# Performance work log

Measured on AMD Instinct MI355X. Metric: run time of the kernel, lower is better.

## Reference

```python
import jax, jax.numpy as jnp
import numpy as np

B, DIM = 8, 2048          # batch, dim == N == C (forced by module's shape constraints)
NUM_HEADS = 8


def setup_inputs() -> dict:
    key = jax.random.key(0)
    k1, k2 = jax.random.split(key)
    x = jax.random.normal(k1, (B, DIM, DIM), dtype=jnp.float32)      # (B, N, C), N==C==dim
    Wq = jax.random.normal(k2, (DIM, DIM), dtype=jnp.float32) * 0.02  # Conv1d(dim,dim,1) weight, no bias
    return {"x": x, "Wq": Wq, "H": 64, "W": 32}


def reference(x, Wq, H, W):
    Bb, N, C = x.shape
    scale = (C // NUM_HEADS) ** -0.5  # qk_scale=None -> head_dim**-0.5
    # self.q: Conv1d(dim, dim, kernel_size=1) applied to x (B, N, C) -> channel axis is N
    q = jnp.einsum('oi,bil->bol', Wq, x)             # (B, N, C)
    # sr_ratio == 1: k_ = x (no spatial reduction; self.sr not constructed)
    attn = jnp.einsum('bnc,bmc->bnm', q, x) * scale  # (B, N, N)
    # self.rwmp = MaxPool1d(dim) with row length N==dim -> max over last axis, keepdim
    m = jnp.max(attn, axis=-1, keepdims=True)        # (B, N, 1)
    # self.v = AvgPool1d(dim) on x^T (B, C, N), N==dim -> mean over tokens
    v = jnp.mean(x, axis=1, keepdims=True)           # (B, 1, C)
    y = m * v                                        # (B, N, 1) @ (B, 1, C) outer product
    # .transpose(1, 2).reshape(B, N, C)  (valid since N == C)
    return jnp.swapaxes(y, 1, 2).reshape(Bb, N, C)
```

## Files before the change

kernel.cpp:

```cpp
#include <hip/hip_runtime.h>

#define DIM 2048
#define NB 8
#define NT (DIM / 64)

typedef _Float16 f16;
typedef __attribute__((ext_vector_type(8))) _Float16 f16x8;
typedef __attribute__((ext_vector_type(4))) _Float16 f16x4;
typedef __attribute__((ext_vector_type(2))) _Float16 f16x2;
typedef __attribute__((ext_vector_type(4))) float f32x4;
typedef __attribute__((ext_vector_type(4))) unsigned u32x4;

__device__ __forceinline__ unsigned fkey(float f) {
    unsigned u = __float_as_uint(f);
    return (u & 0x80000000u) ? ~u : (u | 0x80000000u);
}
__device__ __forceinline__ float fdecode(unsigned k) {
    return (k & 0x80000000u) ? __uint_as_float(k ^ 0x80000000u)
                             : __uint_as_float(~k);
}

__device__ __forceinline__ void gld_lds16(const f16* g, f16* l) {
    __builtin_amdgcn_global_load_lds(
        (const __attribute__((address_space(1))) unsigned*)g,
        (__attribute__((address_space(3))) unsigned*)l, 16, 0, 0);
}

#define BAR() asm volatile("s_barrier" ::: "memory")
#define WAITVM(N) asm volatile("s_waitcnt vmcnt(" #N ")" ::: "memory")

__global__ __launch_bounds__(256) void k_convert(const float* __restrict__ src,
                                                 f16* __restrict__ dst, int n4) {
    int i = blockIdx.x * 256 + threadIdx.x;
    if (i >= n4) return;
    f32x4 v = ((const f32x4*)src)[i];
    ((f16x4*)dst)[i] = __builtin_convertvector(v, f16x4);
}

__global__ __launch_bounds__(256) void k_prep(const float* __restrict__ x,
                                              f16* __restrict__ Xf,
                                              float* __restrict__ vsum) {
    const int b  = blockIdx.z;
    const int c0 = blockIdx.x * 1024 + threadIdx.x * 4;
    const int n0 = blockIdx.y * 64;
    const float* px = x  + ((size_t)b * DIM + n0) * DIM + c0;
    f16*         pd = Xf + ((size_t)b * DIM + n0) * DIM + c0;
    f32x4 s = (f32x4){0.f, 0.f, 0.f, 0.f};
    #pragma unroll 8
    for (int n = 0; n < 64; ++n) {
        f32x4 v = *(const f32x4*)(px + (size_t)n * DIM);
        *(f16x4*)(pd + (size_t)n * DIM) = __builtin_convertvector(v, f16x4);
        s += v;
    }
    atomicAdd(&vsum[b * DIM + c0 + 0], s.x);
    atomicAdd(&vsum[b * DIM + c0 + 1], s.y);
    atomicAdd(&vsum[b * DIM + c0 + 2], s.z);
    atomicAdd(&vsum[b * DIM + c0 + 3], s.w);
}

__global__ __launch_bounds__(256) void k_colsum(const float* __restrict__ x,
                                                float* __restrict__ vsum) {
    int b = blockIdx.z;
    int c = blockIdx.x * 256 + threadIdx.x;
    int n0 = blockIdx.y * (DIM / 8);
    const float* p = x + ((size_t)b * DIM + n0) * DIM + c;
    float s = 0.f;
    #pragma unroll 8
    for (int n = 0; n < DIM / 8; ++n) s += p[(size_t)n * DIM];
    atomicAdd(&vsum[b * DIM + c], s);
}

__device__ __forceinline__ void gemm128_core(const f16* __restrict__ A,
                                             const f16* __restrict__ Bt,
                                             int br, int bc,
                                             f16* As, f16* Bs,
                                             f32x4 acc[4][4]) {
    const int tid  = threadIdx.x;
    const int ln   = tid & 63;
    const int wv   = tid >> 6;
    const int l15  = ln & 15;
    const int quad = ln >> 4;
    const int wr   = (wv >> 1) * 64;
    const int wc   = (wv & 1) * 64;
    const int lrow = ln >> 3;
    const int lg   = (ln & 7) ^ lrow;
    const int swz  = l15 & 7;

    const f16* gA = A  + (size_t)(br * 128 + wv * 32 + lrow) * DIM + lg * 8;
    const f16* gB = Bt + (size_t)(bc * 128 + wv * 32 + lrow) * DIM + lg * 8;
    f16* lA = As + wv * 2048 + ln * 8;
    f16* lB = Bs + wv * 2048 + ln * 8;

    #pragma unroll
    for (int i = 0; i < 4; ++i)
        #pragma unroll
        for (int j = 0; j < 4; ++j)
            acc[i][j] = (f32x4){0.f, 0.f, 0.f, 0.f};

    for (int kt = 0; kt < DIM / 64; ++kt) {
        __syncthreads();
        #pragma unroll
        for (int u = 0; u < 4; ++u) {
            gld_lds16(gA + (size_t)u * 8 * DIM, lA + u * 512);
            gld_lds16(gB + (size_t)u * 8 * DIM, lB + u * 512);
        }
        gA += 64; gB += 64;
        __syncthreads();
        #pragma unroll
        for (int kk = 0; kk < 2; ++kk) {
            const int s = (kk * 4 + quad) ^ swz;
            f16x8 af[4], bf[4];
            #pragma unroll
            for (int i = 0; i < 4; ++i)
                af[i] = *(const f16x8*)(As + (wr + i * 16 + l15) * 64 + s * 8);
            #pragma unroll
            for (int j = 0; j < 4; ++j)
                bf[j] = *(const f16x8*)(Bs + (wc + j * 16 + l15) * 64 + s * 8);
            #pragma unroll
            for (int i = 0; i < 4; ++i)
                #pragma unroll
                for (int j = 0; j < 4; ++j)
                    acc[i][j] = __builtin_amdgcn_mfma_f32_16x16x32_f16(af[i], bf[j], acc[i][j], 0, 0, 0);
        }
    }
}

__global__ __launch_bounds__(256) void k_gram(const f16* __restrict__ Xall,
                                              f16* __restrict__ Gall,
                                              unsigned long xStride,
                                              unsigned long gStride) {
    const int b = blockIdx.y;
    const f16* X = Xall + (size_t)b * xStride;
    f16* G = Gall + (size_t)b * gStride;

    int t = blockIdx.x;
    int br = (int)((sqrtf(8.f * t + 1.f) - 1.f) * 0.5f);
    while ((br + 1) * (br + 2) / 2 <= t) ++br;
    while (br * (br + 1) / 2 > t) --br;
    int bc = t - br * (br + 1) / 2;

    __shared__ __align__(16) f16 smem[128 * 136];
    f16* As = smem;
    f16* Bs = smem + 8192;
    f32x4 acc[4][4];
    gemm128_core(X, X, br, bc, As, Bs, acc);

    const int tid = threadIdx.x;
    const int ln = tid & 63;
    const int wv = tid >> 6;
    const int wr = (wv >> 1) * 64, wc = (wv & 1) * 64;
    const int l15 = ln & 15, quad = ln >> 4;

    #pragma unroll
    for (int i = 0; i < 4; ++i)
        #pragma unroll
        for (int j = 0; j < 4; ++j)
            #pragma unroll
            for (int r = 0; r < 4; ++r) {
                int row = br * 128 + wr + i * 16 + quad * 4 + r;
                int col = bc * 128 + wc + j * 16 + l15;
                G[(size_t)row * DIM + col] = (f16)acc[i][j][r];
            }

    if (br != bc) {
        __syncthreads();
        f16* T = smem;
        #pragma unroll
        for (int i = 0; i < 4; ++i)
            #pragma unroll
            for (int j = 0; j < 4; ++j)
                #pragma unroll
                for (int h = 0; h < 2; ++h) {
                    int row = wr + i * 16 + quad * 4 + h * 2;
                    int col = wc + j * 16 + l15;
                    f16x2 v = {(f16)acc[i][j][h * 2], (f16)acc[i][j][h * 2 + 1]};
                    *(f16x2*)(T + col * 136 + row) = v;
                }
        __syncthreads();
        #pragma unroll
        for (int p = 0; p < 8; ++p) {
            int ch = p * 256 + tid;
            int rt = ch >> 4, seg = ch & 15;
            f16x8 v = *(const f16x8*)(T + rt * 136 + seg * 8);
            *(f16x8*)(G + (size_t)(bc * 128 + rt) * DIM + br * 128 + seg * 8) = v;
        }
    }
}

__global__ __launch_bounds__(512, 2)
void k_attn256(const f16* __restrict__ Wq, const f16* __restrict__ Gall,
               unsigned* __restrict__ mkey, unsigned long gStride, int batchBase) {
    __shared__ __align__(16) f16 sm[2][2][256 * 64];

    const int q  = gridDim.x >> 3;
    const int w  = (blockIdx.x & 7) * q + (blockIdx.x >> 3);
    const int zi = w >> 6;
    const int br = (w >> 3) & 7;
    const int bc = w & 7;
    const f16* A  = Wq;
    const f16* Bt = Gall + (size_t)zi * gStride;
    const int bi = batchBase + zi;

    const int tid  = threadIdx.x;
    const int ln   = tid & 63;
    const int wv   = tid >> 6;
    const int wm   = wv >> 2;
    const int wn   = wv & 3;
    const int l15  = ln & 15;
    const int quad = ln >> 4;
    const int swz  = l15 & 7;
    const int cc0  = ((quad) ^ swz) * 8;
    const int cc1  = ((4 | quad) ^ swz) * 8;
    const int lrow = ln >> 3;
    const int lchunk = (ln & 7) ^ lrow;

    f32x4 acc[8][4];
    #pragma unroll
    for (int i = 0; i < 8; ++i)
        #pragma unroll
        for (int j = 0; j < 4; ++j) acc[i][j] = (f32x4){0.f, 0.f, 0.f, 0.f};

    auto stage = [&](int t, int s) {
        if (t >= NT) return;
        const int p = t & 1;
        const f16* src; int rowb; f16* L;
        if (s == 0 || s == 3) { src = A;  rowb = br * 256; L = (f16*)sm[p][0]; }
        else                  { src = Bt; rowb = bc * 256; L = (f16*)sm[p][1]; }
        const int h  = (s >= 2) ? 1 : 0;
        const int r0 = h * 128 + wv * 16;
        const f16* gp = src + (size_t)(rowb + r0 + lrow) * DIM + t * 64 + lchunk * 8;
        f16* lp = L + r0 * 64 + ln * 8;
        gld_lds16(gp, lp);
        gld_lds16(gp + (size_t)8 * DIM, lp + 512);
    };

    f16x8 af[4][2], bl[2][2], bh[2][2];

    auto loadA = [&](int qm, const f16* LA) {
        #pragma unroll
        for (int i = 0; i < 4; ++i) {
            const f16* pa = LA + (qm * 128 + wm * 64 + i * 16 + l15) * 64;
            af[i][0] = *(const f16x8*)(pa + cc0);
            af[i][1] = *(const f16x8*)(pa + cc1);
        }
    };
    auto loadB = [&](int qn, const f16* LB, f16x8 (&bf)[2][2]) {
        #pragma unroll
        for (int j = 0; j < 2; ++j) {
            const f16* pb = LB + (qn * 128 + wn * 32 + j * 16 + l15) * 64;
            bf[j][0] = *(const f16x8*)(pb + cc0);
            bf[j][1] = *(const f16x8*)(pb + cc1);
        }
    };
    auto mfmaQ = [&](int qm, int qn, f16x8 (&a)[4][2], f16x8 (&bf)[2][2]) {
        __builtin_amdgcn_s_setprio(1);
        #pragma unroll
        for (int i = 0; i < 4; ++i)
            #pragma unroll
            for (int j = 0; j < 2; ++j)
                #pragma unroll
                for (int kk = 0; kk < 2; ++kk)
                    acc[qm * 4 + i][qn * 2 + j] = __builtin_amdgcn_mfma_f32_16x16x32_f16(
                        a[i][kk], bf[j][kk], acc[qm * 4 + i][qn * 2 + j], 0, 0, 0);
        __builtin_amdgcn_s_setprio(0);
    };

    stage(0, 0); stage(0, 1); stage(0, 2); stage(0, 3);
    WAITVM(4);
    stage(1, 0); stage(1, 1); stage(1, 2);
    WAITVM(6);
    BAR();

    for (int t = 0; t < NT; ++t) {
        const f16* LA = (const f16*)sm[t & 1][0];
        const f16* LB = (const f16*)sm[t & 1][1];
        loadA(0, LA); loadB(0, LB, bl); loadB(1, LB, bh);
        stage(t + 1, 3);
        mfmaQ(0, 0, af, bl);
        mfmaQ(0, 1, af, bh);
        BAR();
        loadA(1, LA);
        stage(t + 2, 0); stage(t + 2, 1); stage(t + 2, 2);
        mfmaQ(1, 0, af, bl);
        mfmaQ(1, 1, af, bh);
        if (t < NT - 2) { WAITVM(6); }
        else            { WAITVM(0); }
        BAR();
    }

    const float scale = 0.0625f;
    #pragma unroll
    for (int i = 0; i < 8; ++i) {
        const int qm = i >> 2, il = i & 3;
        #pragma unroll
        for (int r = 0; r < 4; ++r) {
            float v = fmaxf(fmaxf(acc[i][0][r], acc[i][1][r]),
                            fmaxf(acc[i][2][r], acc[i][3][r]));
            #pragma unroll
            for (int m = 1; m <= 8; m <<= 1)
                v = fmaxf(v, __shfl_xor(v, m, 64));
            if (l15 == 0) {
                const int row = br * 256 + qm * 128 + wm * 64 + il * 16 + quad * 4 + r;
                atomicMax(&mkey[(size_t)bi * DIM + row], fkey(scale * v));
            }
        }
    }
}

__global__ __launch_bounds__(256) void k_final(const float* __restrict__ vsum,
                                               const unsigned* __restrict__ mkey,
                                               float* __restrict__ out) {
    int gid = blockIdx.x * 256 + threadIdx.x;
    int b   = gid >> 20;
    int rem = gid & 1048575;
    int i   = rem >> 9;
    int jq  = rem & 511;
    float v = vsum[(b << 11) + i] * (1.f / 2048.f);
    u32x4 k = ((const u32x4*)mkey)[(b << 9) + jq];
    f32x4 o;
    o.x = v * fdecode(k.x);
    o.y = v * fdecode(k.y);
    o.z = v * fdecode(k.z);
    o.w = v * fdecode(k.w);
    ((f32x4*)out)[gid] = o;
}

extern "C" void kernel_launch(void* const* d_in, const int* in_sizes, int n_in,
                              void* d_out, int out_size, void* d_ws, size_t ws_size,
                              hipStream_t stream) {
    const float* x  = (const float*)d_in[0];
    const float* Wq = (const float*)d_in[1];
    float* out = (float*)d_out;
    char* ws = (char*)d_ws;

    const size_t elems = (size_t)DIM * DIM;
    unsigned* mkey = (unsigned*)ws;
    float*    vsum = (float*)(ws + 65536);
    f16*      Wqf  = (f16*)(ws + 131072);
    f16*      Xf   = (f16*)(ws + 131072 + elems * 2);

    const size_t need1 = 131072 + elems * 2 * (1 + NB + NB);
    const size_t need2 = 131072 + elems * 2 * (1 + NB + 1);

    hipMemsetAsync(ws, 0, 131072, stream);
    k_convert<<<4096, 256, 0, stream>>>(Wq, Wqf, (int)(elems / 4));

    if (ws_size >= need1) {
        f16* G = Xf + NB * elems;
        k_prep<<<dim3(2, 32, NB), 256, 0, stream>>>(x, Xf, vsum);
        k_gram<<<dim3(136, NB), 256, 0, stream>>>(Xf, G, elems, elems);
        k_attn256<<<dim3(512), 512, 0, stream>>>(Wqf, G, mkey, elems, 0);
    } else if (ws_size >= need2) {
        f16* G = Xf + NB * elems;
        k_prep<<<dim3(2, 32, NB), 256, 0, stream>>>(x, Xf, vsum);
        for (int b = 0; b < NB; ++b) {
            k_gram<<<dim3(136, 1), 256, 0, stream>>>(Xf + (size_t)b * elems, G, 0, 0);
            k_attn256<<<dim3(64), 512, 0, stream>>>(Wqf, G, mkey, 0, b);
        }
    } else {
        f16* G = Xf + elems;
        k_colsum<<<dim3(8, 8, 8), 256, 0, stream>>>(x, vsum);
        for (int b = 0; b < NB; ++b) {
            k_convert<<<4096, 256, 0, stream>>>(x + (size_t)b * elems, Xf, (int)(elems / 4));
            k_gram<<<dim3(136, 1), 256, 0, stream>>>(Xf, G, 0, 0);
            k_attn256<<<dim3(64), 512, 0, stream>>>(Wqf, G, mkey, 0, b);
        }
    }
    k_final<<<32768, 256, 0, stream>>>(vsum, mkey, out);
}
```

Measured before the change: 485.4 us.

## Double-buffer Gram GEMM LDS loads and split attention launch in two

Replaces the single-buffered Gram kernel with k_gram2. It double-buffers the LDS tiles, prefetching two k-tiles ahead with vmcnt waits, interleaves MFMA halves around the next stage issue, and raises MFMA priority with s_setprio. This aims to hide global-to-LDS load latency behind compute, and launch_bounds(256,2) hints at two blocks per CU. The attention launch is also split into two 256-block launches over batches 0-3 and 4-7, which adds launch overhead. It relies on WAITVM/BAR macros defined elsewhere, and the 64 KB of double-buffered LDS limits occupancy.

```diff
diff --git a/kernel.cpp b/kernel.cpp
--- a/kernel.cpp
+++ b/kernel.cpp
@@ -70,86 +70,98 @@
     atomicAdd(&vsum[b * DIM + c], s);
 }
 
-__device__ __forceinline__ void gemm128_core(const f16* __restrict__ A,
-                                             const f16* __restrict__ Bt,
-                                             int br, int bc,
-                                             f16* As, f16* Bs,
-                                             f32x4 acc[4][4]) {
+__global__ __launch_bounds__(256, 2)
+void k_gram2(const f16* __restrict__ Xall, f16* __restrict__ Gall,
+             unsigned long xStride, unsigned long gStride) {
+    const int b = blockIdx.y;
+    const f16* X = Xall + (size_t)b * xStride;
+    f16* G = Gall + (size_t)b * gStride;
+
+    int t0 = blockIdx.x;
+    int br = (int)((sqrtf(8.f * t0 + 1.f) - 1.f) * 0.5f);
+    while ((br + 1) * (br + 2) / 2 <= t0) ++br;
+    while (br * (br + 1) / 2 > t0) --br;
+    int bc = t0 - br * (br + 1) / 2;
+
+    __shared__ __align__(16) f16 sm[2][2][128 * 64];
+
     const int tid  = threadIdx.x;
     const int ln   = tid & 63;
     const int wv   = tid >> 6;
+    const int wm   = wv >> 1;
+    const int wn   = wv & 1;
     const int l15  = ln & 15;
     const int quad = ln >> 4;
-    const int wr   = (wv >> 1) * 64;
-    const int wc   = (wv & 1) * 64;
+    const int swz  = l15 & 7;
+    const int cc0  = (quad ^ swz) * 8;
+    const int cc1  = ((4 | quad) ^ swz) * 8;
     const int lrow = ln >> 3;
-    const int lg   = (ln & 7) ^ lrow;
-    const int swz  = l15 & 7;
-
-    const f16* gA = A  + (size_t)(br * 128 + wv * 32 + lrow) * DIM + lg * 8;
-    const f16* gB = Bt + (size_t)(bc * 128 + wv * 32 + lrow) * DIM + lg * 8;
-    f16* lA = As + wv * 2048 + ln * 8;
-    f16* lB = Bs + wv * 2048 + ln * 8;
-
+    const int lchunk = (ln & 7) ^ lrow;
+
+    f32x4 acc[4][4];
     #pragma unroll
     for (int i = 0; i < 4; ++i)
         #pragma unroll
-        for (int j = 0; j < 4; ++j)
-            acc[i][j] = (f32x4){0.f, 0.f, 0.f, 0.f};
-
-    for (int kt = 0; kt < DIM / 64; ++kt) {
-        __syncthreads();
-        #pragma unroll
-        for (int u = 0; u < 4; ++u) {
-            gld_lds16(gA + (size_t)u * 8 * DIM, lA + u * 512);
-            gld_lds16(gB + (size_t)u * 8 * DIM, lB + u * 512);
-        }
-        gA += 64; gB += 64;
-        __syncthreads();
-        #pragma unroll
-        for (int kk = 0; kk < 2; ++kk) {
-            const int s = (kk * 4 + quad) ^ swz;
-            f16x8 af[4], bf[4];
-            #pragma unroll
-            for (int i = 0; i < 4; ++i)
-                af[i] = *(const f16x8*)(As + (wr + i * 16 + l15) * 64 + s * 8);
-            #pragma unroll
-            for (int j = 0; j < 4; ++j)
-                bf[j] = *(const f16x8*)(Bs + (wc + j * 16 + l15) * 64 + s * 8);
-            #pragma unroll
-            for (int i = 0; i < 4; ++i)
+        for (int j = 0; j < 4; ++j) acc[i][j] = (f32x4){0.f, 0.f, 0.f, 0.f};
+
+    auto stage = [&](int tt, int op) {
+        if (tt >= NT) return;
+        const int rowb = (op ? bc : br) * 128;
+        const f16* gp = X + (size_t)(rowb + wv * 32 + lrow) * DIM + tt * 64 + lchunk * 8;
+        f16* lp = (f16*)sm[tt & 1][op] + (wv * 32) * 64 + ln * 8;
+        #pragma unroll
+        for (int u = 0; u < 4; ++u)
+            gld_lds16(gp + (size_t)(u * 8) * DIM, lp + u * 512);
+    };
+
+    f16x8 af[4][2], bf[4][2];
+
+    stage(0, 0); stage(0, 1);
+    stage(1, 0); stage(1, 1);
+    WAITVM(8);
+    BAR();
+
+    for (int t = 0; t < NT; ++t) {
+        const f16* LA = (const f16*)sm[t & 1][0];
+        const f16* LB = (const f16*)sm[t & 1][1];
+        #pragma unroll
+        for (int i = 0; i < 4; ++i) {
+            const f16* pa = LA + (wm * 64 + i * 16 + l15) * 64;
+            af[i][0] = *(const f16x8*)(pa + cc0);
+            af[i][1] = *(const f16x8*)(pa + cc1);
+        }
+        #pragma unroll
+        for (int j = 0; j < 4; ++j) {
+            const f16* pb = LB + (wn * 64 + j * 16 + l15) * 64;
+            bf[j][0] = *(const f16x8*)(pb + cc0);
+            bf[j][1] = *(const f16x8*)(pb + cc1);
+        }
+        __builtin_amdgcn_s_setprio(1);
+        #pragma unroll
+        for (int i = 0; i < 4; ++i)
+            #pragma unroll
+            for (int j = 0; j < 2; ++j)
                 #pragma unroll
-                for (int j = 0; j < 4; ++j)
-                    acc[i][j] = __builtin_amdgcn_mfma_f32_16x16x32_f16(af[i], bf[j], acc[i][j], 0, 0, 0);
-        }
-    }
-}
-
-__global__ __launch_bounds__(256) void k_gram(const f16* __restrict__ Xall,
-                                              f16* __restrict__ Gall,
-                                              unsigned long xStride,
-                                              unsigned long gStride) {
-    const int b = blockIdx.y;
-    const f16* X = Xall + (size_t)b * xStride;
-    f16* G = Gall + (size_t)b * gStride;
-
-    int t = blockIdx.x;
-    int br = (int)((sqrtf(8.f * t + 1.f) - 1.f) * 0.5f);
-    while ((br + 1) * (br + 2) / 2 <= t) ++br;
-    while (br * (br + 1) / 2 > t) --br;
-    int bc = t - br * (br + 1) / 2;
-
-    __shared__ __align__(16) f16 smem[128 * 136];
-    f16* As = smem;
-    f16* Bs = smem + 8192;
-    f32x4 acc[4][4];
-    gemm128_core(X, X, br, bc, As, Bs, acc);
-
-    const int tid = threadIdx.x;
-    const int ln = tid & 63;
-    const int wv = tid >> 6;
-    const int wr = (wv >> 1) * 64, wc = (wv & 1) * 64;
-    const int l15 = ln & 15, quad = ln >> 4;
+                for (int kk = 0; kk < 2; ++kk)
+                    acc[i][j] = __builtin_amdgcn_mfma_f32_16x16x32_f16(af[i][kk], bf[j][kk], acc[i][j], 0, 0, 0);
+        __builtin_amdgcn_s_setprio(0);
+        BAR();
+        stage(t + 2, 0); stage(t + 2, 1);
+        __builtin_amdgcn_s_setprio(1);
+        #pragma unroll
+        for (int i = 0; i < 4; ++i)
+            #pragma unroll
+            for (int j = 2; j < 4; ++j)
+                #pragma unroll
+                for (int kk = 0; kk < 2; ++kk)
+                    acc[i][j] = __builtin_amdgcn_mfma_f32_16x16x32_f16(af[i][kk], bf[j][kk], acc[i][j], 0, 0, 0);
+        __builtin_amdgcn_s_setprio(0);
+        if (t < NT - 2) { WAITVM(8); }
+        else            { WAITVM(0); }
+        BAR();
+    }
+
+    const int wr = wm * 64, wc = wn * 64;
 
     #pragma unroll
     for (int i = 0; i < 4; ++i)
@@ -164,7 +176,7 @@
 
     if (br != bc) {
         __syncthreads();
-        f16* T = smem;
+        f16* T = (f16*)sm;
         #pragma unroll
         for (int i = 0; i < 4; ++i)
             #pragma unroll
@@ -348,13 +360,14 @@
     if (ws_size >= need1) {
         f16* G = Xf + NB * elems;
         k_prep<<<dim3(2, 32, NB), 256, 0, stream>>>(x, Xf, vsum);
-        k_gram<<<dim3(136, NB), 256, 0, stream>>>(Xf, G, elems, elems);
-        k_attn256<<<dim3(512), 512, 0, stream>>>(Wqf, G, mkey, elems, 0);
+        k_gram2<<<dim3(136, NB), 256, 0, stream>>>(Xf, G, elems, elems);
+        k_attn256<<<dim3(256), 512, 0, stream>>>(Wqf, G, mkey, elems, 0);
+        k_attn256<<<dim3(256), 512, 0, stream>>>(Wqf, G + (size_t)4 * elems, mkey, elems, 4);
     } else if (ws_size >= need2) {
         f16* G = Xf + NB * elems;
         k_prep<<<dim3(2, 32, NB), 256, 0, stream>>>(x, Xf, vsum);
         for (int b = 0; b < NB; ++b) {
-            k_gram<<<dim3(136, 1), 256, 0, stream>>>(Xf + (size_t)b * elems, G, 0, 0);
+            k_gram2<<<dim3(136, 1), 256, 0, stream>>>(Xf + (size_t)b * elems, G, 0, 0);
             k_attn256<<<dim3(64), 512, 0, stream>>>(Wqf, G, mkey, 0, b);
         }
     } else {
@@ -362,7 +375,7 @@
         k_colsum<<<dim3(8, 8, 8), 256, 0, stream>>>(x, vsum);
         for (int b = 0; b < NB; ++b) {
             k_convert<<<4096, 256, 0, stream>>>(x + (size_t)b * elems, Xf, (int)(elems / 4));
-            k_gram<<<dim3(136, 1), 256, 0, stream>>>(Xf, G, 0, 0);
+            k_gram2<<<dim3(136, 1), 256, 0, stream>>>(Xf, G, 0, 0);
             k_attn256<<<dim3(64), 512, 0, stream>>>(Wqf, G, mkey, 0, b);
         }
     }
```

After: 490.4 us. Within noise of the previous version (+1.0%).
